# Kernel tuning notes

Measured on AMD Instinct MI355X. Metric: run time of the kernel, lower is better.

## Reference

```python
import jax, jax.numpy as jnp
import numpy as np
from functools import partial

# Mask R-CNN inference-config constants
BBOX_STD_DEV = jnp.array([0.1, 0.1, 0.2, 0.2], dtype=jnp.float32)
DETECTION_MIN_CONFIDENCE = 0.7
DETECTION_NMS_THRESHOLD = 0.3
DETECTION_MAX_INSTANCES = 100
NUM_CLASSES = 81
CLASS_OFFSET = 2.0  # > max extent of normalized boxes -> zero cross-class IoU


def setup_inputs() -> dict:
    key = jax.random.key(0)
    k1, k2, k3, k4 = jax.random.split(key, 4)
    B, N, C = 8, 2000, NUM_CLASSES
    # normalized rois with y1<y2, x1<x2
    yx = jax.random.uniform(k1, (B, N, 2)) * 0.7
    hw = jax.random.uniform(k2, (B, N, 2)) * 0.25 + 0.01
    rois = jnp.concatenate([yx, yx + hw], axis=-1)
    # peaked class probabilities so many rois exceed the 0.7 confidence floor
    mrcnn_class = jax.nn.softmax(jax.random.normal(k3, (B, N, C)) * 5.0, axis=-1)
    mrcnn_bbox = jax.random.normal(k4, (B, N, C, 4)) * 0.5
    meta = np.zeros((B, 12 + C), dtype=np.float32)
    meta[:, 1:4] = [1024.0, 1024.0, 3.0]   # original_image_shape
    meta[:, 4:7] = [1024.0, 1024.0, 3.0]   # image_shape
    meta[:, 7:11] = [0.0, 0.0, 1024.0, 1024.0]  # window in pixels
    meta[:, 11] = 1.0                       # scale
    meta[:, 12:] = 1.0                      # active_class_ids
    return {"rois": rois, "mrcnn_class": mrcnn_class,
            "mrcnn_bbox": mrcnn_bbox, "image_meta": jnp.asarray(meta)}


def _apply_box_deltas(boxes, deltas):
    h = boxes[:, 2] - boxes[:, 0]
    w = boxes[:, 3] - boxes[:, 1]
    cy = boxes[:, 0] + 0.5 * h + deltas[:, 0] * h
    cx = boxes[:, 1] + 0.5 * w + deltas[:, 1] * w
    h = h * jnp.exp(deltas[:, 2])
    w = w * jnp.exp(deltas[:, 3])
    y1 = cy - 0.5 * h
    x1 = cx - 0.5 * w
    return jnp.stack([y1, x1, y1 + h, x1 + w], axis=1)


def _clip_boxes(boxes, window):
    wy1, wx1, wy2, wx2 = window[0], window[1], window[2], window[3]
    y1 = jnp.clip(boxes[:, 0], wy1, wy2)
    x1 = jnp.clip(boxes[:, 1], wx1, wx2)
    y2 = jnp.clip(boxes[:, 2], wy1, wy2)
    x2 = jnp.clip(boxes[:, 3], wx1, wx2)
    return jnp.stack([y1, x1, y2, x2], axis=1)


def _iou_matrix(b):
    y1, x1, y2, x2 = b[:, 0], b[:, 1], b[:, 2], b[:, 3]
    area = (y2 - y1) * (x2 - x1)
    ih = jnp.clip(jnp.minimum(y2[:, None], y2[None, :]) - jnp.maximum(y1[:, None], y1[None, :]), 0.0)
    iw = jnp.clip(jnp.minimum(x2[:, None], x2[None, :]) - jnp.maximum(x1[:, None], x1[None, :]), 0.0)
    inter = ih * iw
    union = area[:, None] + area[None, :] - inter
    return inter / (union + 1e-8)


def _refine_detections(rois, probs, deltas, window):
    N = probs.shape[0]
    class_ids = jnp.argmax(probs, axis=1)                       # [N]
    rng = jnp.arange(N)
    class_scores = probs[rng, class_ids]
    deltas_specific = deltas[rng, class_ids]                    # [N,4]
    refined = _apply_box_deltas(rois, deltas_specific * BBOX_STD_DEV)
    refined = _clip_boxes(refined, window)
    valid = (class_ids > 0) & (class_scores >= DETECTION_MIN_CONFIDENCE)
    # sort by score desc (invalid pushed to the end)
    order = jnp.argsort(-jnp.where(valid, class_scores, -1.0))
    boxes_s = refined[order]
    # per-class NMS via class-offset trick: IoU across classes is exactly 0
    offset = class_ids[order].astype(refined.dtype)[:, None] * CLASS_OFFSET
    iou = jax.lax.stop_gradient(_iou_matrix(boxes_s + offset))
    keep0 = valid[order]
    idxs = jnp.arange(N)

    def body(i, keep):
        sup = (iou[i] > DETECTION_NMS_THRESHOLD) & keep[i] & (idxs > i)
        return keep & ~sup

    keep = jax.lax.fori_loop(0, N, body, keep0)
    sel_scores = jnp.where(keep, class_scores[order], -1.0)
    top_vals, top_i = jax.lax.top_k(sel_scores, DETECTION_MAX_INSTANCES)
    mask = (top_vals >= 0.0).astype(refined.dtype)[:, None]
    idx = order[top_i]
    det = jnp.concatenate([
        refined[idx],
        class_ids[idx].astype(refined.dtype)[:, None],
        class_scores[idx][:, None],
    ], axis=1)
    return det * mask                                           # [100,6], zero-padded


def reference(rois, mrcnn_class, mrcnn_bbox, image_meta):
    image_shape = image_meta[0, 4:7]
    h, w = image_shape[0], image_shape[1]
    scale = jnp.stack([h, w, h, w]) - 1.0
    shift = jnp.array([0.0, 0.0, 1.0, 1.0], dtype=image_meta.dtype)
    window = (image_meta[:, 7:11] - shift) / scale              # [B,4] normalized
    return jax.vmap(_refine_detections)(rois, mrcnn_class, mrcnn_bbox, window)
```

## Files before the change

### kernel.cpp

```cpp
#include <hip/hip_runtime.h>
#include <cfloat>
#include <cmath>

#define NROI 2000
#define NCLS 81
#define META 93
#define NMS_TAU 0.3f
#define MINCONF 0.7f
#define MAXDET 100
#define SORTN 2048

typedef unsigned long long u64;


__global__ __launch_bounds__(256) void refine_kernel(const float* __restrict__ rois,
                                                     const float* __restrict__ probs,
                                                     const float* __restrict__ deltas,
                                                     const float* __restrict__ meta,
                                                     float4* __restrict__ wbox,
                                                     u64* __restrict__ wpack,
                                                     int total) {
#pragma clang fp contract(off)
    const int tid = threadIdx.x;
    const int r = tid & 7;
    const int t = blockIdx.x * 32 + (tid >> 3);
    if (t >= total) return;
    const int b = t / NROI;
    const int j = t - b * NROI;

    const float* p = probs + (size_t)t * NCLS;
    float best = p[r];
    int bi = r;
    for (int c = r + 8; c < NCLS; c += 8) {
        float v = p[c];
        if (v > best) { best = v; bi = c; }
    }
    for (int m = 1; m < 8; m <<= 1) {
        float v2 = __shfl_xor(best, m);
        int i2 = __shfl_xor(bi, m);
        if (v2 > best || (v2 == best && i2 < bi)) { best = v2; bi = i2; }
    }
    if (r != 0) return;

    const float* dp = deltas + ((size_t)t * NCLS + bi) * 4;
    float4 dd = *(const float4*)dp;
    float d0 = dd.x * 0.1f, d1 = dd.y * 0.1f, d2 = dd.z * 0.2f, d3 = dd.w * 0.2f;
    float4 rr = *(const float4*)(rois + (size_t)t * 4);
    float r0 = rr.x, r1 = rr.y, r2 = rr.z, r3 = rr.w;
    float h = r2 - r0, w = r3 - r1;
    float cy = (r0 + 0.5f * h) + d0 * h;
    float cx = (r1 + 0.5f * w) + d1 * w;
    float h2 = h * expf(d2);
    float w2 = w * expf(d3);
    float y1 = cy - 0.5f * h2, x1 = cx - 0.5f * w2;
    float y2 = y1 + h2, x2 = x1 + w2;

    const float sy = meta[4] - 1.0f;
    const float sx = meta[5] - 1.0f;
    const float* mb = meta + (size_t)b * META;
    const float wy1 = (mb[7] - 0.0f) / sy;
    const float wx1 = (mb[8] - 0.0f) / sx;
    const float wy2 = (mb[9] - 1.0f) / sy;
    const float wx2 = (mb[10] - 1.0f) / sx;
    y1 = fminf(fmaxf(y1, wy1), wy2);
    x1 = fminf(fmaxf(x1, wx1), wx2);
    y2 = fminf(fmaxf(y2, wy1), wy2);
    x2 = fminf(fmaxf(x2, wx1), wx2);

    bool valid = (bi > 0) && (best >= MINCONF);
    float key = valid ? best : -1.0f;
    unsigned kb = __float_as_uint(key);
    unsigned ip = (kb & 0x80000000u) ? ~kb : (kb | 0x80000000u);
    unsigned dk = ~ip;
    wbox[t] = make_float4(y1, x1, y2, x2);
    wpack[(size_t)b * SORTN + j] = ((u64)dk << 32) | (unsigned)(j << 7) | (unsigned)bi;
}

__global__ __launch_bounds__(512) void sort512_kernel(u64* __restrict__ wpack) {
    __shared__ u64 sp[512];
    const int bc = blockIdx.x;
    const int b = bc >> 2, chunk = bc & 3;
    const int base = chunk * 512;
    const int tid = threadIdx.x;

    {
        int j = base + tid;
        sp[tid] = (j < NROI) ? wpack[(size_t)b * SORTN + j]
                             : (0xC000000000000000ull | (u64)((unsigned)j << 7));
    }
    __syncthreads();

    for (int k = 2; k <= 256; k <<= 1) {
        for (int jj = k >> 1; jj > 0; jj >>= 1) {
            int i = tid, ixj = tid ^ jj;
            if (ixj > i) {
                u64 pa = sp[i], pb = sp[ixj];
                bool asc = ((i & k) == 0);
                if ((pa > pb) == asc) { sp[i] = pb; sp[ixj] = pa; }
            }
            __syncthreads();
        }
    }
    for (int jj = 256; jj > 0; jj >>= 1) {
        int i = tid, ixj = tid ^ jj;
        if (ixj > i) {
            u64 pa = sp[i], pb = sp[ixj];
            if (pa > pb) { sp[i] = pb; sp[ixj] = pa; }
        }
        __syncthreads();
    }
    wpack[(size_t)b * SORTN + base + tid] = sp[tid];
}

__global__ __launch_bounds__(1024) void merge_nms_kernel(const float4* __restrict__ wbox,
                                                         const u64* __restrict__ wpack,
                                                         float* __restrict__ out) {
#pragma clang fp contract(off)
    __shared__ u64 s_pack[SORTN];
    __shared__ float4 s_boxArena[NROI];
    __shared__ unsigned char s_keep[SORTN];
    __shared__ float s_cy1[64], s_cx1[64], s_cy2[64], s_cx2[64], s_car[64];
    __shared__ int s_ccl[64], s_init[64];
    __shared__ u64 s_sup[64];
    __shared__ u64 s_alive;
    __shared__ int s_scan[17];
    __shared__ int s_total, s_V;

    u64* s_tmp = (u64*)s_boxArena;
    float4* s_box = s_boxArena;

    const int b = blockIdx.x;
    const int tid = threadIdx.x;

    for (int j = tid; j < SORTN; j += 1024)
        s_pack[j] = wpack[(size_t)b * SORTN + j];
    __syncthreads();

    for (int i = tid; i < SORTN; i += 1024) {
        u64 x = s_pack[i];
        int run = i >> 9, local = i & 511;
        int pbase = (run ^ 1) << 9;
        int lo = 0, hi = 512;
        while (lo < hi) {
            int mid = (lo + hi) >> 1;
            if (s_pack[pbase + mid] < x) lo = mid + 1; else hi = mid;
        }
        s_tmp[((run >> 1) << 10) + local + lo] = x;
    }
    __syncthreads();

    for (int i = tid; i < SORTN; i += 1024) {
        u64 x = s_tmp[i];
        int run = i >> 10, local = i & 1023;
        int pbase = (run ^ 1) << 10;
        int lo = 0, hi = 1024;
        while (lo < hi) {
            int mid = (lo + hi) >> 1;
            if (s_tmp[pbase + mid] < x) lo = mid + 1; else hi = mid;
        }
        s_pack[local + lo] = x;
    }
    __syncthreads();

    for (int j = tid; j < NROI; j += 1024)
        s_box[j] = wbox[b * NROI + j];
    if (tid == 0) {
        int lo = 0, hi = SORTN;
        while (lo < hi) {
            int mid = (lo + hi) >> 1;
            if (!(s_pack[mid] >> 63)) lo = mid + 1; else hi = mid;
        }
        s_V = lo;
        s_total = 0;
    }
    __syncthreads();
    const int V = s_V;
    for (int j = tid; j < SORTN; j += 1024) s_keep[j] = (j < V) ? 1 : 0;
    __syncthreads();

    for (int c = 0; c < V; c += 64) {
        bool init_flag = false;
        if (tid < 64) {
            int j = c + tid;
            int cl = -1;
            float y1 = 0.f, x1 = 0.f, y2 = 0.f, x2 = 0.f, ar = 0.f;
            if (j < V) {
                init_flag = (s_keep[j] != 0);
                u64 pk = s_pack[j];
                int o = (int)((pk >> 7) & 0x7FF);
                cl = (int)(pk & 0x7F);
                float4 bx = s_box[o];
                float off = (float)cl * 2.0f;
                y1 = bx.x + off; x1 = bx.y + off; y2 = bx.z + off; x2 = bx.w + off;
                ar = (y2 - y1) * (x2 - x1);
            }
            s_cy1[tid] = y1; s_cx1[tid] = x1; s_cy2[tid] = y2; s_cx2[tid] = x2;
            s_car[tid] = ar; s_ccl[tid] = cl; s_init[tid] = init_flag ? 1 : 0;
        }
        __syncthreads();

        {
            int i = tid & 63;
            int w = tid >> 6;
            float iy1 = s_cy1[i], ix1 = s_cx1[i], iy2 = s_cy2[i], ix2 = s_cx2[i];
            float iar = s_car[i];
            int icl = s_ccl[i], iin = s_init[i];
#pragma unroll
            for (int p = 0; p < 4; ++p) {
                int jr = w + (p << 4);
                float jy1 = s_cy1[jr], jx1 = s_cx1[jr], jy2 = s_cy2[jr], jx2 = s_cx2[jr];
                float jar = s_car[jr];
                int jcl = s_ccl[jr], jin = s_init[jr];
                bool bit = false;
                if (i < jr && iin && jin && icl == jcl) {
                    float ih = fmaxf(fminf(jy2, iy2) - fmaxf(jy1, iy1), 0.0f);
                    float iw = fmaxf(fminf(jx2, ix2) - fmaxf(jx1, ix1), 0.0f);
                    float inter = ih * iw;
                    float iou = inter / ((jar + iar - inter) + 1e-8f);
                    bit = iou > NMS_TAU;
                }
                u64 m = __ballot(bit);
                if (i == 0) s_sup[jr] = m;
            }
        }
        __syncthreads();

        if (tid < 64) {
            u64 sup = s_sup[tid];
            u64 initm = __ballot(init_flag);
            u64 hasup = __ballot(init_flag && sup != 0ull);
            u64 alive = initm & ~hasup;
            u64 m = hasup;
            while (m) {
                int t2 = __ffsll((unsigned long long)m) - 1;
                m &= m - 1;
                u64 st = __shfl(sup, t2);
                if ((st & alive) == 0ull) alive |= (1ull << t2);
            }
            s_keep[c + tid] = (unsigned char)((alive >> tid) & 1ull);
            if (tid == 0) { s_alive = alive; s_total += __popcll(alive); }
        }
        __syncthreads();
        if (s_total >= MAXDET) break;

        u64 alive = s_alive;
        if (alive) {
            for (int j = c + 64 + tid; j < V; j += 1024) {
                if (!s_keep[j]) continue;
                u64 pk = s_pack[j];
                int o = (int)((pk >> 7) & 0x7FF);
                int myc = (int)(pk & 0x7F);
                float4 bx = s_box[o];
                float off = (float)myc * 2.0f;
                float y1 = bx.x + off, x1 = bx.y + off, y2 = bx.z + off, x2 = bx.w + off;
                float ar = (y2 - y1) * (x2 - x1);
                int keep = 1;
                u64 m = alive;
                while (m) {
                    int kI = __ffsll((unsigned long long)m) - 1;
                    m &= m - 1;
                    if (s_ccl[kI] != myc) continue;
                    float iy1 = s_cy1[kI], ix1 = s_cx1[kI];
                    float iy2 = s_cy2[kI], ix2 = s_cx2[kI];
                    float iar = s_car[kI];
                    float ih = fmaxf(fminf(y2, iy2) - fmaxf(y1, iy1), 0.0f);
                    float iw = fmaxf(fminf(x2, ix2) - fmaxf(x1, ix1), 0.0f);
                    float inter = ih * iw;
                    float iou = inter / ((ar + iar - inter) + 1e-8f);
                    if (iou > NMS_TAU) { keep = 0; break; }
                }
                if (!keep) s_keep[j] = 0;
            }
        }
        __syncthreads();
    }
    __syncthreads();

    int a0 = (int)s_keep[2 * tid], a1 = (int)s_keep[2 * tid + 1];
    int ssum = a0 + a1;
    int lane = tid & 63, wid = tid >> 6;
    int v = ssum;
    for (int off = 1; off < 64; off <<= 1) {
        int n = __shfl_up(v, off);
        if (lane >= off) v += n;
    }
    if (lane == 63) s_scan[wid] = v;
    __syncthreads();
    if (tid == 0) {
        int acc = 0;
        for (int wv = 0; wv < 16; ++wv) { int t2 = s_scan[wv]; s_scan[wv] = acc; acc += t2; }
        s_scan[16] = acc;
    }
    __syncthreads();
    int incl = v + s_scan[wid];
    int excl0 = incl - ssum;
    int excl1 = excl0 + a0;

    float* ob = out + (size_t)b * (MAXDET * 6);
    for (int e = 0; e < 2; ++e) {
        int j = 2 * tid + e;
        int kp = e ? a1 : a0;
        int rk = e ? excl1 : excl0;
        if (kp && rk < MAXDET) {
            u64 pk = s_pack[j];
            int o = (int)((pk >> 7) & 0x7FF);
            int cl = (int)(pk & 0x7F);
            unsigned ip = ~(unsigned)(pk >> 32);
            unsigned kb = (ip & 0x80000000u) ? (ip & 0x7FFFFFFFu) : ~ip;
            float4 bx = s_box[o];
            float* row = ob + rk * 6;
            row[0] = bx.x; row[1] = bx.y; row[2] = bx.z; row[3] = bx.w;
            row[4] = (float)cl;
            row[5] = __uint_as_float(kb);
        }
    }
    int K = s_scan[16];
    if (K > MAXDET) K = MAXDET;
    for (int s0 = K + tid; s0 < MAXDET; s0 += 1024) {
        float* row = ob + s0 * 6;
#pragma unroll
        for (int q = 0; q < 6; ++q) row[q] = 0.0f;
    }
}

__global__ __launch_bounds__(1024) void det_kernel(const float* __restrict__ rois,
                                                   const float* __restrict__ probs,
                                                   const float* __restrict__ deltas,
                                                   const float* __restrict__ meta,
                                                   float* __restrict__ out) {
#pragma clang fp contract(off)
    __shared__ float s_key[SORTN];
    __shared__ unsigned short s_idx[SORTN];
    __shared__ float4 s_box[NROI];
    __shared__ unsigned char s_cls[NROI];
    __shared__ unsigned char s_keep[SORTN];
    __shared__ float s_chunk[64 * 5];
    __shared__ int s_scan[17];
    __shared__ int s_nk, s_total, s_V;

    const int b = blockIdx.x;
    const int tid = threadIdx.x;

    const float sy = meta[4] - 1.0f;
    const float sx = meta[5] - 1.0f;
    const float* mb = meta + (size_t)b * META;
    const float wy1 = (mb[7] - 0.0f) / sy;
    const float wx1 = (mb[8] - 0.0f) / sx;
    const float wy2 = (mb[9] - 1.0f) / sy;
    const float wx2 = (mb[10] - 1.0f) / sx;

    for (int j = tid; j < SORTN; j += 1024) {
        s_idx[j] = (unsigned short)j;
        if (j >= NROI) { s_key[j] = -2.0f; continue; }
        const int t = b * NROI + j;
        const float* p = probs + (size_t)t * NCLS;
        float best = p[0];
        int bi = 0;
        for (int c = 1; c < NCLS; ++c) {
            float v = p[c];
            if (v > best) { best = v; bi = c; }
        }
        const float* dp = deltas + ((size_t)t * NCLS + bi) * 4;
        float d0 = dp[0] * 0.1f, d1 = dp[1] * 0.1f, d2 = dp[2] * 0.2f, d3 = dp[3] * 0.2f;
        const float* rp = rois + (size_t)t * 4;
        float r0 = rp[0], r1 = rp[1], r2 = rp[2], r3 = rp[3];
        float h = r2 - r0, w = r3 - r1;
        float cy = (r0 + 0.5f * h) + d0 * h;
        float cx = (r1 + 0.5f * w) + d1 * w;
        float h2 = h * expf(d2);
        float w2 = w * expf(d3);
        float y1 = cy - 0.5f * h2, x1 = cx - 0.5f * w2;
        float y2 = y1 + h2, x2 = x1 + w2;
        y1 = fminf(fmaxf(y1, wy1), wy2);
        x1 = fminf(fmaxf(x1, wx1), wx2);
        y2 = fminf(fmaxf(y2, wy1), wy2);
        x2 = fminf(fmaxf(x2, wx1), wx2);
        bool valid = (bi > 0) && (best >= MINCONF);
        s_key[j] = valid ? best : -1.0f;
        s_box[j] = make_float4(y1, x1, y2, x2);
        s_cls[j] = (unsigned char)bi;
    }
    __syncthreads();

    for (int k = 2; k <= SORTN; k <<= 1) {
        for (int jj = k >> 1; jj > 0; jj >>= 1) {
            for (int i = tid; i < SORTN; i += 1024) {
                int ixj = i ^ jj;
                if (ixj > i) {
                    float ka = s_key[i], kb = s_key[ixj];
                    unsigned short ia = s_idx[i], ib = s_idx[ixj];
                    bool b_prec_a = (kb > ka) || (kb == ka && ib < ia);
                    bool dir = ((i & k) == 0);
                    if (b_prec_a == dir) {
                        s_key[i] = kb; s_key[ixj] = ka;
                        s_idx[i] = ib; s_idx[ixj] = ia;
                    }
                }
            }
            __syncthreads();
        }
    }

    if (tid == 0) {
        int lo = 0, hi = SORTN;
        while (lo < hi) {
            int mid = (lo + hi) >> 1;
            if (s_key[mid] > 0.0f) lo = mid + 1; else hi = mid;
        }
        s_V = lo;
        s_total = 0;
    }
    __syncthreads();
    const int V = s_V;

    for (int j = tid; j < SORTN; j += 1024) s_keep[j] = (j < V) ? 1 : 0;
    __syncthreads();

    for (int c = 0; c < V; c += 64) {
        if (tid < 64) {
            int j = c + tid;
            int keep = 0;
            float y1 = 0.f, x1 = 0.f, y2 = 0.f, x2 = 0.f, ar = 0.f;
            if (j < V) {
                keep = (int)s_keep[j];
                int o = (int)s_idx[j];
                float4 bx = s_box[o];
                float off = (float)s_cls[o] * 2.0f;
                y1 = bx.x + off; x1 = bx.y + off; y2 = bx.z + off; x2 = bx.w + off;
                ar = (y2 - y1) * (x2 - x1);
            }
            for (int i = 0; i < 63; ++i) {
                int ki = __shfl(keep, i);
                float iy1 = __shfl(y1, i), ix1 = __shfl(x1, i);
                float iy2 = __shfl(y2, i), ix2 = __shfl(x2, i);
                float iar = __shfl(ar, i);
                if (tid > i && keep && ki) {
                    float ih = fmaxf(fminf(y2, iy2) - fmaxf(y1, iy1), 0.0f);
                    float iw = fmaxf(fminf(x2, ix2) - fmaxf(x1, ix1), 0.0f);
                    float inter = ih * iw;
                    float iou = inter / ((ar + iar - inter) + 1e-8f);
                    if (iou > NMS_TAU) keep = 0;
                }
            }
            if (j < V) s_keep[j] = (unsigned char)keep;
            unsigned long long bal = __ballot(keep && (j < V));
            int nk = __popcll(bal);
            if (keep && j < V) {
                int pos = __popcll(bal & ((1ULL << tid) - 1ULL));
                s_chunk[pos * 5 + 0] = y1; s_chunk[pos * 5 + 1] = x1;
                s_chunk[pos * 5 + 2] = y2; s_chunk[pos * 5 + 3] = x2;
                s_chunk[pos * 5 + 4] = ar;
            }
            if (tid == 0) { s_nk = nk; s_total += nk; }
        }
        __syncthreads();
        if (s_total >= MAXDET) break;
        int nk = s_nk;
        if (nk > 0) {
            for (int j = c + 64 + tid; j < V; j += 1024) {
                if (!s_keep[j]) continue;
                int o = (int)s_idx[j];
                float4 bx = s_box[o];
                float off = (float)s_cls[o] * 2.0f;
                float y1 = bx.x + off, x1 = bx.y + off, y2 = bx.z + off, x2 = bx.w + off;
                float ar = (y2 - y1) * (x2 - x1);
                int keep = 1;
                for (int kI = 0; kI < nk; ++kI) {
                    float iy1 = s_chunk[kI * 5 + 0], ix1 = s_chunk[kI * 5 + 1];
                    float iy2 = s_chunk[kI * 5 + 2], ix2 = s_chunk[kI * 5 + 3];
                    float iar = s_chunk[kI * 5 + 4];
                    float ih = fmaxf(fminf(y2, iy2) - fmaxf(y1, iy1), 0.0f);
                    float iw = fmaxf(fminf(x2, ix2) - fmaxf(x1, ix1), 0.0f);
                    float inter = ih * iw;
                    float iou = inter / ((ar + iar - inter) + 1e-8f);
                    if (iou > NMS_TAU) { keep = 0; break; }
                }
                if (!keep) s_keep[j] = 0;
            }
        }
        __syncthreads();
    }
    __syncthreads();

    int a0 = (int)s_keep[2 * tid], a1 = (int)s_keep[2 * tid + 1];
    int ssum = a0 + a1;
    int lane = tid & 63, wid = tid >> 6;
    int v = ssum;
    for (int off = 1; off < 64; off <<= 1) {
        int n = __shfl_up(v, off);
        if (lane >= off) v += n;
    }
    if (lane == 63) s_scan[wid] = v;
    __syncthreads();
    if (tid == 0) {
        int acc = 0;
        for (int wv = 0; wv < 16; ++wv) { int t2 = s_scan[wv]; s_scan[wv] = acc; acc += t2; }
        s_scan[16] = acc;
    }
    __syncthreads();
    int incl = v + s_scan[wid];
    int excl0 = incl - ssum;
    int excl1 = excl0 + a0;

    float* ob = out + (size_t)b * (MAXDET * 6);
    for (int e = 0; e < 2; ++e) {
        int j = 2 * tid + e;
        int kp = e ? a1 : a0;
        int rk = e ? excl1 : excl0;
        if (kp && rk < MAXDET) {
            int o = (int)s_idx[j];
            float4 bx = s_box[o];
            float* row = ob + rk * 6;
            row[0] = bx.x; row[1] = bx.y; row[2] = bx.z; row[3] = bx.w;
            row[4] = (float)s_cls[o];
            row[5] = s_key[j];
        }
    }
    int K = s_scan[16];
    if (K > MAXDET) K = MAXDET;
    for (int s0 = K + tid; s0 < MAXDET; s0 += 1024) {
        float* row = ob + s0 * 6;
#pragma unroll
        for (int q = 0; q < 6; ++q) row[q] = 0.0f;
    }
}

extern "C" void kernel_launch(void* const* d_in, const int* in_sizes, int n_in,
                              void* d_out, int out_size, void* d_ws, size_t ws_size,
                              hipStream_t stream) {
    const float* rois   = (const float*)d_in[0];
    const float* probs  = (const float*)d_in[1];
    const float* deltas = (const float*)d_in[2];
    const float* meta   = (const float*)d_in[3];
    float* out = (float*)d_out;

    int B = in_sizes[0] / (NROI * 4);
    int total = B * NROI;

    size_t need = (size_t)total * 16 + (size_t)B * SORTN * 8;
    if (ws_size >= need) {
        float4* wbox = (float4*)d_ws;
        u64*    wpack = (u64*)(wbox + total);
        refine_kernel<<<(total + 31) / 32, 256, 0, stream>>>(rois, probs, deltas, meta,
                                                             wbox, wpack, total);
        sort512_kernel<<<B * 4, 512, 0, stream>>>(wpack);
        merge_nms_kernel<<<B, 1024, 0, stream>>>(wbox, wpack, out);
    } else {
        det_kernel<<<B, 1024, 0, stream>>>(rois, probs, deltas, meta, out);
    }
}
```

Baseline: 106.0 us.

## Use register bitonic sort with shuffles and per-class alive masks in NMS

The 512-element bitonic sort now keeps each element in a register. Strides below 64 are exchanged with wavefront shuffles, so only the large strides go through shared memory and need barriers. The NMS suppression loop now builds a per-class bitmask of surviving boxes for each 64-box chunk, so a candidate only checks same-class survivors and skips the loop entirely when there are none. The box loads are also issued early into registers to overlap the global-memory latency with the merge phase. The cost is extra atomics to build the masks and two barriers per large-stride sort step.

```diff
diff --git a/kernel.cpp b/kernel.cpp
--- a/kernel.cpp
+++ b/kernel.cpp
@@ -83,33 +83,29 @@
     const int base = chunk * 512;
     const int tid = threadIdx.x;
 
-    {
-        int j = base + tid;
-        sp[tid] = (j < NROI) ? wpack[(size_t)b * SORTN + j]
-                             : (0xC000000000000000ull | (u64)((unsigned)j << 7));
-    }
-    __syncthreads();
-
-    for (int k = 2; k <= 256; k <<= 1) {
+    int j = base + tid;
+    u64 v = (j < NROI) ? wpack[(size_t)b * SORTN + j]
+                       : (0xC000000000000000ull | (u64)((unsigned)j << 7));
+
+    for (int k = 2; k <= 512; k <<= 1) {
+        const bool asc = ((tid & k) == 0);
         for (int jj = k >> 1; jj > 0; jj >>= 1) {
-            int i = tid, ixj = tid ^ jj;
-            if (ixj > i) {
-                u64 pa = sp[i], pb = sp[ixj];
-                bool asc = ((i & k) == 0);
-                if ((pa > pb) == asc) { sp[i] = pb; sp[ixj] = pa; }
-            }
-            __syncthreads();
-        }
-    }
-    for (int jj = 256; jj > 0; jj >>= 1) {
-        int i = tid, ixj = tid ^ jj;
-        if (ixj > i) {
-            u64 pa = sp[i], pb = sp[ixj];
-            if (pa > pb) { sp[i] = pb; sp[ixj] = pa; }
-        }
-        __syncthreads();
-    }
-    wpack[(size_t)b * SORTN + base + tid] = sp[tid];
+            u64 pv;
+            if (jj >= 64) {
+                sp[tid] = v;
+                __syncthreads();
+                pv = sp[tid ^ jj];
+                __syncthreads();
+            } else {
+                pv = __shfl_xor(v, jj);
+            }
+            bool lower = ((tid & jj) == 0);
+            bool keepmin = (lower == asc);
+            bool vless = (v < pv);
+            v = (keepmin == vless) ? v : pv;
+        }
+    }
+    wpack[(size_t)b * SORTN + base + tid] = v;
 }
 
 __global__ __launch_bounds__(1024) void merge_nms_kernel(const float4* __restrict__ wbox,
@@ -122,6 +118,7 @@
     __shared__ float s_cy1[64], s_cx1[64], s_cy2[64], s_cx2[64], s_car[64];
     __shared__ int s_ccl[64], s_init[64];
     __shared__ u64 s_sup[64];
+    __shared__ u64 s_clsmask[NCLS];
     __shared__ u64 s_alive;
     __shared__ int s_scan[17];
     __shared__ int s_total, s_V;
@@ -131,6 +128,11 @@
 
     const int b = blockIdx.x;
     const int tid = threadIdx.x;
+
+    float4 rb0 = wbox[b * NROI + tid];
+    float4 rb1;
+    const int bj1 = tid + 1024;
+    if (bj1 < NROI) rb1 = wbox[b * NROI + bj1];
 
     for (int j = tid; j < SORTN; j += 1024)
         s_pack[j] = wpack[(size_t)b * SORTN + j];
@@ -162,8 +164,8 @@
     }
     __syncthreads();
 
-    for (int j = tid; j < NROI; j += 1024)
-        s_box[j] = wbox[b * NROI + j];
+    s_box[tid] = rb0;
+    if (bj1 < NROI) s_box[bj1] = rb1;
     if (tid == 0) {
         int lo = 0, hi = SORTN;
         while (lo < hi) {
@@ -196,6 +198,8 @@
             }
             s_cy1[tid] = y1; s_cx1[tid] = x1; s_cy2[tid] = y2; s_cx2[tid] = x2;
             s_car[tid] = ar; s_ccl[tid] = cl; s_init[tid] = init_flag ? 1 : 0;
+        } else if (tid >= 64 && tid < 64 + NCLS) {
+            s_clsmask[tid - 64] = 0ull;
         }
         __syncthreads();
 
@@ -238,28 +242,29 @@
                 if ((st & alive) == 0ull) alive |= (1ull << t2);
             }
             s_keep[c + tid] = (unsigned char)((alive >> tid) & 1ull);
+            if ((alive >> tid) & 1ull)
+                atomicOr(&s_clsmask[s_ccl[tid]], 1ull << tid);
             if (tid == 0) { s_alive = alive; s_total += __popcll(alive); }
         }
         __syncthreads();
         if (s_total >= MAXDET) break;
 
-        u64 alive = s_alive;
-        if (alive) {
+        if (s_alive) {
             for (int j = c + 64 + tid; j < V; j += 1024) {
                 if (!s_keep[j]) continue;
                 u64 pk = s_pack[j];
+                int myc = (int)(pk & 0x7F);
+                u64 m = s_clsmask[myc];
+                if (!m) continue;
                 int o = (int)((pk >> 7) & 0x7FF);
-                int myc = (int)(pk & 0x7F);
                 float4 bx = s_box[o];
                 float off = (float)myc * 2.0f;
                 float y1 = bx.x + off, x1 = bx.y + off, y2 = bx.z + off, x2 = bx.w + off;
                 float ar = (y2 - y1) * (x2 - x1);
                 int keep = 1;
-                u64 m = alive;
                 while (m) {
                     int kI = __ffsll((unsigned long long)m) - 1;
                     m &= m - 1;
-                    if (s_ccl[kI] != myc) continue;
                     float iy1 = s_cy1[kI], ix1 = s_cx1[kI];
                     float iy2 = s_cy2[kI], ix2 = s_cx2[kI];
                     float iar = s_car[kI];
```

Result: faster. 94.79 us (-10.6%).
